# Optimization experiments

Hardware: AMD Instinct MI355X
Metric: run time of the kernel (lower is better)

The kernel has to match this reference:

```python
import jax, jax.numpy as jnp
import numpy as np

EPS = 1e-12  # torch F.normalize eps


def setup_inputs() -> dict:
    key = jax.random.key(0)
    k1, k2, k3 = jax.random.split(key, 3)
    b, c, h, w = 4, 192, 128, 128
    num_heads = 8
    in1 = jax.random.normal(k1, (b, c, h, w), dtype=jnp.float32)
    in2 = jax.random.normal(k2, (b, c, h, w), dtype=jnp.float32)
    scale = jnp.ones((num_heads, 1, 1), dtype=jnp.float32)
    proj_w = jax.random.normal(k3, (c, c), dtype=jnp.float32) * (1.0 / np.sqrt(c))
    return {"in1": in1, "in2": in2, "scale": scale, "proj_w": proj_w, "num_heads": num_heads}


def reference(in1, in2, scale, proj_w, num_heads):
    b, c, h, w = in1.shape
    hd = c // num_heads
    hw = h * w
    # b (head c) h w -> b head c (h w)
    q = in1.reshape(b, num_heads, hd, hw)
    k = in2.reshape(b, num_heads, hd, hw)
    # L2-normalize along the (h w) axis, torch eps semantics
    q = q / jnp.maximum(jnp.linalg.norm(q, axis=-1, keepdims=True), EPS)
    k = k / jnp.maximum(jnp.linalg.norm(k, axis=-1, keepdims=True), EPS)
    # channel-wise attention: [b, head, c, c]
    attn = jnp.einsum('bhcn,bhdn->bhcd', q, k) * scale  # scale broadcasts [head,1,1]
    attn = jax.nn.softmax(attn, axis=-1)
    out = jnp.einsum('bhcd,bhdn->bhcn', attn, k)
    out = out.reshape(b, c, h, w)
    # 1x1 conv projection (no bias)
    out = jnp.einsum('oc,bchw->bohw', proj_w, out)
    return out
```

## Files before the change

### kernel.cpp

```cpp
#include <hip/hip_runtime.h>
#include <hip/hip_bf16.h>
#include <math.h>

#define BATCH 4
#define NHEAD 8
#define HD 24
#define CH 192
#define HW 16384
#define SPL 32
#define SROW 640

#define OFF_MO  (32 * SPL * SROW)
#define OFF_CNT (OFF_MO + (BATCH * CH * CH) / 2)

#define LSTR 132

typedef __attribute__((ext_vector_type(8)))  short bf16x8;
typedef __attribute__((ext_vector_type(16))) float f32x16;

__device__ __forceinline__ unsigned short bf16rne(float x) {
    union { float f; unsigned u; } v; v.f = x;
    unsigned u = v.u;
    return (unsigned short)((u + 0x7FFFu + ((u >> 16) & 1u)) >> 16);
}

__device__ __forceinline__ unsigned pack2(float a, float b) {
    union { __hip_bfloat162 h; unsigned u; } c;
    c.h = __float22bfloat162_rn(float2{a, b});
    return c.u;
}

__device__ __forceinline__ void st_agent(float* p, float v) {
    __hip_atomic_store(p, v, __ATOMIC_RELAXED, __HIP_MEMORY_SCOPE_AGENT);
}
__device__ __forceinline__ float ld_agent(const float* p) {
    return __hip_atomic_load(p, __ATOMIC_RELAXED, __HIP_MEMORY_SCOPE_AGENT);
}

__global__ __launch_bounds__(256, 4) void kA(const float* __restrict__ q,
                                             const float* __restrict__ k,
                                             const float* __restrict__ scale,
                                             const float* __restrict__ w,
                                             float* __restrict__ ws,
                                             unsigned short* __restrict__ Mo,
                                             unsigned int* __restrict__ cnt) {
    __shared__ unsigned int tile[2][HD * LSTR];
    __shared__ int lastFlag;

    const int bh   = blockIdx.x;
    const int ch   = blockIdx.y;
    const int t    = threadIdx.x;
    const int lane = t & 63;
    const int wave = t >> 6;
    const int m    = lane & 31;
    const int hi   = lane >> 5;
    const int rowc = (m < HD) ? m : 0;

    f32x16 aQK = {}, aQQ = {}, aKK = {};

    #pragma unroll
    for (int half = 0; half < 2; ++half) {
        const float* qb = q + (size_t)bh * HD * HW + ch * 512 + half * 256;
        const float* kb = k + (size_t)bh * HD * HW + ch * 512 + half * 256;

        #pragma unroll
        for (int j = 0; j < 6; ++j) {
            const int idx = j * 256 + t;
            const int row = idx >> 6;
            const int c64 = idx & 63;
            float4 qv = *(const float4*)(qb + (size_t)row * HW + c64 * 4);
            float4 kv = *(const float4*)(kb + (size_t)row * HW + c64 * 4);
            *(uint2*)&tile[0][row * LSTR + c64 * 2] =
                make_uint2(pack2(qv.x, qv.y), pack2(qv.z, qv.w));
            *(uint2*)&tile[1][row * LSTR + c64 * 2] =
                make_uint2(pack2(kv.x, kv.y), pack2(kv.z, kv.w));
        }
        __syncthreads();

        #pragma unroll
        for (int s = 0; s < 4; ++s) {
            const int off = (wave * 64 + s * 16) >> 1;
            bf16x8 aq = *(const bf16x8*)&tile[0][rowc * LSTR + off + hi * 4];
            bf16x8 bk = *(const bf16x8*)&tile[1][rowc * LSTR + off + hi * 4];
            aQK = __builtin_amdgcn_mfma_f32_32x32x16_bf16(aq, bk, aQK, 0, 0, 0);
            aQQ = __builtin_amdgcn_mfma_f32_32x32x16_bf16(aq, aq, aQQ, 0, 0, 0);
            aKK = __builtin_amdgcn_mfma_f32_32x32x16_bf16(bk, bk, aKK, 0, 0, 0);
        }
        __syncthreads();
    }

    float* red = (float*)tile;
    if (m < HD) {
        #pragma unroll
        for (int r = 0; r < 16; ++r) {
            const int i = (r & 3) + 8 * (r >> 2) + 4 * hi;
            if (i < HD) {
                red[wave * 624 + i * HD + m] = aQK[r];
                if (i == m) {
                    red[wave * 624 + 576 + i] = aQQ[r];
                    red[wave * 624 + 600 + i] = aKK[r];
                }
            }
        }
    }
    __syncthreads();

    float* Srow = ws + ((size_t)bh * SPL + ch) * SROW;
    for (int e = t; e < 624; e += 256)
        st_agent(&Srow[e], red[e] + red[624 + e] + red[1248 + e] + red[1872 + e]);

    asm volatile("s_waitcnt vmcnt(0)" ::: "memory");
    __syncthreads();

    if (t == 0) {
        unsigned int old = __hip_atomic_fetch_add(&cnt[bh], 1u,
                                                  __ATOMIC_RELAXED,
                                                  __HIP_MEMORY_SCOPE_AGENT);
        lastFlag = (old == SPL - 1);
    }
    __syncthreads();
    if (!lastFlag) return;

    float* sf = (float*)tile;
    const int b = bh >> 3;
    const int h = bh & 7;
    const float* base = ws + (size_t)bh * SPL * SROW;

    for (int idx = t; idx < CH * HD; idx += 256) {
        int o = idx / HD, dd = idx - o * HD;
        sf[672 + idx] = w[o * CH + h * HD + dd];
    }
    for (int e = t; e < 624; e += 256) {
        float s0 = 0.f, s1 = 0.f, s2 = 0.f, s3 = 0.f;
        #pragma unroll
        for (int sp = 0; sp < SPL; sp += 4) {
            s0 += ld_agent(&base[(size_t)(sp + 0) * SROW + e]);
            s1 += ld_agent(&base[(size_t)(sp + 1) * SROW + e]);
            s2 += ld_agent(&base[(size_t)(sp + 2) * SROW + e]);
            s3 += ld_agent(&base[(size_t)(sp + 3) * SROW + e]);
        }
        sf[e] = (s0 + s1) + (s2 + s3);
    }
    __syncthreads();

    if (t < 2 * HD) {
        float inv = 1.0f / fmaxf(sqrtf(sf[576 + t]), 1e-12f);
        sf[624 + t] = inv;
    }
    __syncthreads();

    const float sc = scale[h];
    for (int e = t; e < 576; e += 256)
        sf[e] = sf[e] * sf[624 + e / HD] * sf[648 + e % HD] * sc;
    __syncthreads();

    if (t < HD) {
        float mx = -1e30f;
        for (int j = 0; j < HD; ++j) mx = fmaxf(mx, sf[t * HD + j]);
        float sum = 0.f;
        for (int j = 0; j < HD; ++j) {
            float v = expf(sf[t * HD + j] - mx);
            sf[t * HD + j] = v;
            sum += v;
        }
        float r = 1.0f / sum;
        for (int j = 0; j < HD; ++j) sf[t * HD + j] *= r;
    }
    __syncthreads();

    for (int idx = t; idx < CH * HD; idx += 256) {
        int o = idx / HD, j = idx - o * HD;
        float v = 0.f;
        #pragma unroll
        for (int i = 0; i < HD; ++i)
            v = fmaf(sf[672 + o * HD + i], sf[i * HD + j], v);
        Mo[(size_t)b * CH * CH + (size_t)o * CH + h * HD + j] = bf16rne(v * sf[648 + j]);
    }
}

#define KCN 64
#define BSTR3 100

__global__ __launch_bounds__(256, 4) void kC(const float* __restrict__ k,
                                             const unsigned short* __restrict__ Mo,
                                             float* __restrict__ out) {
    __shared__ unsigned int Bt[KCN * BSTR3];

    const int t    = threadIdx.x;
    const int lane = t & 63;
    const int wave = t >> 6;
    const int n31  = lane & 31;
    const int hi   = lane >> 5;
    const int nt   = wave & 1;
    const int otb  = (wave >> 1) * 3;

    const int nb = blockIdx.x * KCN;
    const int b  = blockIdx.y;

    const float* kb = k + (size_t)b * CH * HW;
    const unsigned short* Mob = Mo + (size_t)b * CH * CH;

    const int np4 = t & 15;
    const int cg4 = t >> 4;

    #pragma unroll
    for (int s = 0; s < 3; ++s) {
        float4 v[4];
        #pragma unroll
        for (int cc = 0; cc < 4; ++cc)
            v[cc] = *(const float4*)(kb + (size_t)(s * 64 + cg4 * 4 + cc) * HW + nb + np4 * 4);
        #pragma unroll
        for (int r = 0; r < 4; ++r) {
            float x0 = (&v[0].x)[r], x1 = (&v[1].x)[r];
            float x2 = (&v[2].x)[r], x3 = (&v[3].x)[r];
            *(uint2*)&Bt[(np4 * 4 + r) * BSTR3 + s * 32 + cg4 * 2] =
                make_uint2(pack2(x0, x1), pack2(x2, x3));
        }
    }
    __syncthreads();

    f32x16 acc[3] = {};
    #pragma unroll
    for (int kc = 0; kc < 12; ++kc) {
        bf16x8 Bf = *(const bf16x8*)&Bt[(nt * 32 + n31) * BSTR3 + kc * 8 + hi * 4];
        #pragma unroll
        for (int oi = 0; oi < 3; ++oi) {
            const unsigned short* ap =
                Mob + (size_t)((otb + oi) * 32 + n31) * CH + kc * 16 + hi * 8;
            bf16x8 Af = *(const bf16x8*)ap;
            acc[oi] = __builtin_amdgcn_mfma_f32_32x32x16_bf16(Af, Bf, acc[oi], 0, 0, 0);
        }
    }

    float* op = out + (size_t)b * CH * HW;
    const int n = nb + nt * 32 + n31;
    #pragma unroll
    for (int oi = 0; oi < 3; ++oi)
        #pragma unroll
        for (int r = 0; r < 16; ++r) {
            int o = (otb + oi) * 32 + (r & 3) + 8 * (r >> 2) + 4 * hi;
            op[(size_t)o * HW + n] = acc[oi][r];
        }
}

extern "C" void kernel_launch(void* const* d_in, const int* in_sizes, int n_in,
                              void* d_out, int out_size, void* d_ws, size_t ws_size,
                              hipStream_t stream) {
    const float* in1   = (const float*)d_in[0];
    const float* in2   = (const float*)d_in[1];
    const float* scale = (const float*)d_in[2];
    const float* projw = (const float*)d_in[3];
    float* ws  = (float*)d_ws;
    float* out = (float*)d_out;
    unsigned short* Mo = (unsigned short*)(ws + OFF_MO);
    unsigned int* cnt  = (unsigned int*)(ws + OFF_CNT);

    hipMemsetAsync((void*)cnt, 0, 32 * sizeof(unsigned int), stream);
    kA<<<dim3(32, SPL), 256, 0, stream>>>(in1, in2, scale, projw, ws, Mo, cnt);
    kC<<<dim3(HW / KCN, BATCH), 256, 0, stream>>>(in2, Mo, out);
}
```

Measured before the change: 174.4 us.

## Software-pipeline global loads with smaller LDS chunks in both kernels

Both kernels now register-prefetch the next chunk of global input while the current chunk is packed to LDS and consumed by MFMAs, instead of loading everything up front and then computing. kA splits its 512-column slice into four 128-column chunks with a smaller LDS tile, and kC streams the 192-channel reduction in three 64-channel stages with a smaller transpose buffer. The aim is to overlap memory latency with compute and to shrink LDS use so more blocks can be resident. In exchange there are more barriers per block and extra live registers for the prefetch buffers.

```diff
diff --git a/kernel.cpp b/kernel.cpp
--- a/kernel.cpp
+++ b/kernel.cpp
@@ -13,7 +13,9 @@
 #define OFF_MO  (32 * SPL * SROW)
 #define OFF_CNT (OFF_MO + (BATCH * CH * CH) / 2)
 
-#define LSTR 132
+#define CHK  128
+#define NCHK 4
+#define ASTR 66
 
 typedef __attribute__((ext_vector_type(8)))  short bf16x8;
 typedef __attribute__((ext_vector_type(16))) float f32x16;
@@ -44,11 +46,12 @@
                                              float* __restrict__ ws,
                                              unsigned short* __restrict__ Mo,
                                              unsigned int* __restrict__ cnt) {
-    __shared__ unsigned int tile[2][HD * LSTR];
+    __shared__ float smem[5280];
+    unsigned int* tile = (unsigned int*)smem;
     __shared__ int lastFlag;
 
     const int bh   = blockIdx.x;
-    const int ch   = blockIdx.y;
+    const int cb   = blockIdx.y;
     const int t    = threadIdx.x;
     const int lane = t & 63;
     const int wave = t >> 6;
@@ -56,40 +59,59 @@
     const int hi   = lane >> 5;
     const int rowc = (m < HD) ? m : 0;
 
+    const float* qb = q + (size_t)bh * HD * HW + cb * 512;
+    const float* kb = k + (size_t)bh * HD * HW + cb * 512;
+
+    int rowj[3], c4j[3];
+    #pragma unroll
+    for (int j = 0; j < 3; ++j) {
+        const int idx = j * 256 + t;
+        rowj[j] = idx >> 5;
+        c4j[j]  = idx & 31;
+    }
+
+    float4 vq[3], vk[3];
+    #pragma unroll
+    for (int j = 0; j < 3; ++j) {
+        vq[j] = *(const float4*)(qb + (size_t)rowj[j] * HW + c4j[j] * 4);
+        vk[j] = *(const float4*)(kb + (size_t)rowj[j] * HW + c4j[j] * 4);
+    }
+
     f32x16 aQK = {}, aQQ = {}, aKK = {};
 
     #pragma unroll
-    for (int half = 0; half < 2; ++half) {
-        const float* qb = q + (size_t)bh * HD * HW + ch * 512 + half * 256;
-        const float* kb = k + (size_t)bh * HD * HW + ch * 512 + half * 256;
-
-        #pragma unroll
-        for (int j = 0; j < 6; ++j) {
-            const int idx = j * 256 + t;
-            const int row = idx >> 6;
-            const int c64 = idx & 63;
-            float4 qv = *(const float4*)(qb + (size_t)row * HW + c64 * 4);
-            float4 kv = *(const float4*)(kb + (size_t)row * HW + c64 * 4);
-            *(uint2*)&tile[0][row * LSTR + c64 * 2] =
-                make_uint2(pack2(qv.x, qv.y), pack2(qv.z, qv.w));
-            *(uint2*)&tile[1][row * LSTR + c64 * 2] =
-                make_uint2(pack2(kv.x, kv.y), pack2(kv.z, kv.w));
+    for (int c = 0; c < NCHK; ++c) {
+        if (c) __syncthreads();
+
+        #pragma unroll
+        for (int j = 0; j < 3; ++j) {
+            *(uint2*)&tile[rowj[j] * ASTR + c4j[j] * 2] =
+                make_uint2(pack2(vq[j].x, vq[j].y), pack2(vq[j].z, vq[j].w));
+            *(uint2*)&tile[24 * ASTR + rowj[j] * ASTR + c4j[j] * 2] =
+                make_uint2(pack2(vk[j].x, vk[j].y), pack2(vk[j].z, vk[j].w));
+        }
+        if (c + 1 < NCHK) {
+            #pragma unroll
+            for (int j = 0; j < 3; ++j) {
+                vq[j] = *(const float4*)(qb + (size_t)rowj[j] * HW + (c + 1) * CHK + c4j[j] * 4);
+                vk[j] = *(const float4*)(kb + (size_t)rowj[j] * HW + (c + 1) * CHK + c4j[j] * 4);
+            }
         }
         __syncthreads();
 
         #pragma unroll
-        for (int s = 0; s < 4; ++s) {
-            const int off = (wave * 64 + s * 16) >> 1;
-            bf16x8 aq = *(const bf16x8*)&tile[0][rowc * LSTR + off + hi * 4];
-            bf16x8 bk = *(const bf16x8*)&tile[1][rowc * LSTR + off + hi * 4];
+        for (int s = 0; s < 2; ++s) {
+            const int off = wave * 16 + s * 8;
+            bf16x8 aq = *(const bf16x8*)&tile[rowc * ASTR + off + hi * 4];
+            bf16x8 bk = *(const bf16x8*)&tile[24 * ASTR + rowc * ASTR + off + hi * 4];
             aQK = __builtin_amdgcn_mfma_f32_32x32x16_bf16(aq, bk, aQK, 0, 0, 0);
             aQQ = __builtin_amdgcn_mfma_f32_32x32x16_bf16(aq, aq, aQQ, 0, 0, 0);
             aKK = __builtin_amdgcn_mfma_f32_32x32x16_bf16(bk, bk, aKK, 0, 0, 0);
         }
-        __syncthreads();
-    }
-
-    float* red = (float*)tile;
+    }
+    __syncthreads();
+
+    float* red = smem;
     if (m < HD) {
         #pragma unroll
         for (int r = 0; r < 16; ++r) {
@@ -105,7 +127,7 @@
     }
     __syncthreads();
 
-    float* Srow = ws + ((size_t)bh * SPL + ch) * SROW;
+    float* Srow = ws + ((size_t)bh * SPL + cb) * SROW;
     for (int e = t; e < 624; e += 256)
         st_agent(&Srow[e], red[e] + red[624 + e] + red[1248 + e] + red[1872 + e]);
 
@@ -121,7 +143,7 @@
     __syncthreads();
     if (!lastFlag) return;
 
-    float* sf = (float*)tile;
+    float* sf = smem;
     const int b = bh >> 3;
     const int h = bh & 7;
     const float* base = ws + (size_t)bh * SPL * SROW;
@@ -179,12 +201,12 @@
 }
 
 #define KCN 64
-#define BSTR3 100
+#define BSTR2 36
 
 __global__ __launch_bounds__(256, 4) void kC(const float* __restrict__ k,
                                              const unsigned short* __restrict__ Mo,
                                              float* __restrict__ out) {
-    __shared__ unsigned int Bt[KCN * BSTR3];
+    __shared__ unsigned int Bt[KCN * BSTR2];
 
     const int t    = threadIdx.x;
     const int lane = t & 63;
@@ -201,34 +223,43 @@
     const unsigned short* Mob = Mo + (size_t)b * CH * CH;
 
     const int np4 = t & 15;
-    const int cg4 = t >> 4;
+    const int cg  = t >> 4;
+
+    float4 v[4];
+    #pragma unroll
+    for (int cc = 0; cc < 4; ++cc)
+        v[cc] = *(const float4*)(kb + (size_t)(cg * 4 + cc) * HW + nb + np4 * 4);
+
+    f32x16 acc[3] = {};
 
     #pragma unroll
     for (int s = 0; s < 3; ++s) {
-        float4 v[4];
-        #pragma unroll
-        for (int cc = 0; cc < 4; ++cc)
-            v[cc] = *(const float4*)(kb + (size_t)(s * 64 + cg4 * 4 + cc) * HW + nb + np4 * 4);
+        if (s) __syncthreads();
+
         #pragma unroll
         for (int r = 0; r < 4; ++r) {
             float x0 = (&v[0].x)[r], x1 = (&v[1].x)[r];
             float x2 = (&v[2].x)[r], x3 = (&v[3].x)[r];
-            *(uint2*)&Bt[(np4 * 4 + r) * BSTR3 + s * 32 + cg4 * 2] =
+            *(uint2*)&Bt[(np4 * 4 + r) * BSTR2 + cg * 2] =
                 make_uint2(pack2(x0, x1), pack2(x2, x3));
         }
-    }
-    __syncthreads();
-
-    f32x16 acc[3] = {};
-    #pragma unroll
-    for (int kc = 0; kc < 12; ++kc) {
-        bf16x8 Bf = *(const bf16x8*)&Bt[(nt * 32 + n31) * BSTR3 + kc * 8 + hi * 4];
-        #pragma unroll
-        for (int oi = 0; oi < 3; ++oi) {
-            const unsigned short* ap =
-                Mob + (size_t)((otb + oi) * 32 + n31) * CH + kc * 16 + hi * 8;
-            bf16x8 Af = *(const bf16x8*)ap;
-            acc[oi] = __builtin_amdgcn_mfma_f32_32x32x16_bf16(Af, Bf, acc[oi], 0, 0, 0);
+        if (s + 1 < 3) {
+            #pragma unroll
+            for (int cc = 0; cc < 4; ++cc)
+                v[cc] = *(const float4*)(kb + (size_t)((s + 1) * 64 + cg * 4 + cc) * HW + nb + np4 * 4);
+        }
+        __syncthreads();
+
+        #pragma unroll
+        for (int kc = 0; kc < 4; ++kc) {
+            bf16x8 Bf = *(const bf16x8*)&Bt[(nt * 32 + n31) * BSTR2 + kc * 8 + hi * 4];
+            #pragma unroll
+            for (int oi = 0; oi < 3; ++oi) {
+                const unsigned short* ap =
+                    Mob + (size_t)((otb + oi) * 32 + n31) * CH + s * 64 + kc * 16 + hi * 8;
+                bf16x8 Af = *(const bf16x8*)ap;
+                acc[oi] = __builtin_amdgcn_mfma_f32_32x32x16_bf16(Af, Bf, acc[oi], 0, 0, 0);
+            }
         }
     }
 
```

Result: no change. 175.8 us (+0.8%).

## Enlarge tiles in both kernels and stage output through LDS for coalesced stores

Applied to the files above, without the earlier changes.

kA now processes 1024 columns per block with half as many splits, and its loads are reorganised so each wave fetches whole rows of q/k into one shared arena. kC grows to 256 columns per block with 512 threads, reloads the k slice in three 64-channel stages, and computes all 192 output rows per wave. Results are transposed through LDS so the output is written as coalesced float4 rows instead of scattered scalar stores. The aim is fewer blocks, more reuse of the Mo loads per block, and better global write efficiency, at the cost of extra barriers and fewer resident blocks per CU.

```diff
diff --git a/kernel.cpp b/kernel.cpp
--- a/kernel.cpp
+++ b/kernel.cpp
@@ -7,13 +7,13 @@
 #define HD 24
 #define CH 192
 #define HW 16384
-#define SPL 32
+#define SPL 16
 #define SROW 640
 
 #define OFF_MO  (32 * SPL * SROW)
 #define OFF_CNT (OFF_MO + (BATCH * CH * CH) / 2)
 
-#define LSTR 132
+#define ASTR 260
 
 typedef __attribute__((ext_vector_type(8)))  short bf16x8;
 typedef __attribute__((ext_vector_type(16))) float f32x16;
@@ -37,18 +37,18 @@
     return __hip_atomic_load(p, __ATOMIC_RELAXED, __HIP_MEMORY_SCOPE_AGENT);
 }
 
-__global__ __launch_bounds__(256, 4) void kA(const float* __restrict__ q,
+__global__ __launch_bounds__(256, 2) void kA(const float* __restrict__ q,
                                              const float* __restrict__ k,
                                              const float* __restrict__ scale,
                                              const float* __restrict__ w,
                                              float* __restrict__ ws,
                                              unsigned short* __restrict__ Mo,
                                              unsigned int* __restrict__ cnt) {
-    __shared__ unsigned int tile[2][HD * LSTR];
+    __shared__ unsigned int arena[48 * ASTR];
     __shared__ int lastFlag;
 
     const int bh   = blockIdx.x;
-    const int ch   = blockIdx.y;
+    const int cb   = blockIdx.y;
     const int t    = threadIdx.x;
     const int lane = t & 63;
     const int wave = t >> 6;
@@ -56,40 +56,54 @@
     const int hi   = lane >> 5;
     const int rowc = (m < HD) ? m : 0;
 
+    const float* qb = q + (size_t)bh * HD * HW + cb * 1024;
+    const float* kb = k + (size_t)bh * HD * HW + cb * 1024;
+
     f32x16 aQK = {}, aQQ = {}, aKK = {};
 
     #pragma unroll
     for (int half = 0; half < 2; ++half) {
-        const float* qb = q + (size_t)bh * HD * HW + ch * 512 + half * 256;
-        const float* kb = k + (size_t)bh * HD * HW + ch * 512 + half * 256;
-
-        #pragma unroll
-        for (int j = 0; j < 6; ++j) {
-            const int idx = j * 256 + t;
-            const int row = idx >> 6;
-            const int c64 = idx & 63;
-            float4 qv = *(const float4*)(qb + (size_t)row * HW + c64 * 4);
-            float4 kv = *(const float4*)(kb + (size_t)row * HW + c64 * 4);
-            *(uint2*)&tile[0][row * LSTR + c64 * 2] =
-                make_uint2(pack2(qv.x, qv.y), pack2(qv.z, qv.w));
-            *(uint2*)&tile[1][row * LSTR + c64 * 2] =
-                make_uint2(pack2(kv.x, kv.y), pack2(kv.z, kv.w));
-        }
-        __syncthreads();
-
-        #pragma unroll
-        for (int s = 0; s < 4; ++s) {
-            const int off = (wave * 64 + s * 16) >> 1;
-            bf16x8 aq = *(const bf16x8*)&tile[0][rowc * LSTR + off + hi * 4];
-            bf16x8 bk = *(const bf16x8*)&tile[1][rowc * LSTR + off + hi * 4];
+        if (half) __syncthreads();
+
+        #pragma unroll
+        for (int grp = 0; grp < 3; ++grp) {
+            float4 v[8];
+            #pragma unroll
+            for (int rr = 0; rr < 4; ++rr) {
+                const int r48 = wave * 12 + grp * 4 + rr;
+                const float* src = (r48 < 24) ? qb : kb;
+                const int row = (r48 < 24) ? r48 : r48 - 24;
+                #pragma unroll
+                for (int i = 0; i < 2; ++i)
+                    v[rr * 2 + i] = *(const float4*)(src + (size_t)row * HW +
+                                                     half * 512 + i * 256 + lane * 4);
+            }
+            #pragma unroll
+            for (int rr = 0; rr < 4; ++rr) {
+                const int r48 = wave * 12 + grp * 4 + rr;
+                #pragma unroll
+                for (int i = 0; i < 2; ++i) {
+                    float4 x = v[rr * 2 + i];
+                    *(uint2*)&arena[r48 * ASTR + i * 128 + lane * 2] =
+                        make_uint2(pack2(x.x, x.y), pack2(x.z, x.w));
+                }
+            }
+        }
+        __syncthreads();
+
+        #pragma unroll
+        for (int s = 0; s < 8; ++s) {
+            const int k16 = wave * 8 + s;
+            bf16x8 aq = *(const bf16x8*)&arena[rowc * ASTR + k16 * 8 + hi * 4];
+            bf16x8 bk = *(const bf16x8*)&arena[(24 + rowc) * ASTR + k16 * 8 + hi * 4];
             aQK = __builtin_amdgcn_mfma_f32_32x32x16_bf16(aq, bk, aQK, 0, 0, 0);
             aQQ = __builtin_amdgcn_mfma_f32_32x32x16_bf16(aq, aq, aQQ, 0, 0, 0);
             aKK = __builtin_amdgcn_mfma_f32_32x32x16_bf16(bk, bk, aKK, 0, 0, 0);
         }
-        __syncthreads();
-    }
-
-    float* red = (float*)tile;
+    }
+    __syncthreads();
+
+    float* red = (float*)arena;
     if (m < HD) {
         #pragma unroll
         for (int r = 0; r < 16; ++r) {
@@ -105,7 +119,7 @@
     }
     __syncthreads();
 
-    float* Srow = ws + ((size_t)bh * SPL + ch) * SROW;
+    float* Srow = ws + ((size_t)bh * SPL + cb) * SROW;
     for (int e = t; e < 624; e += 256)
         st_agent(&Srow[e], red[e] + red[624 + e] + red[1248 + e] + red[1872 + e]);
 
@@ -121,7 +135,7 @@
     __syncthreads();
     if (!lastFlag) return;
 
-    float* sf = (float*)tile;
+    float* sf = (float*)arena;
     const int b = bh >> 3;
     const int h = bh & 7;
     const float* base = ws + (size_t)bh * SPL * SROW;
@@ -178,21 +192,20 @@
     }
 }
 
-#define KCN 64
-#define BSTR3 100
-
-__global__ __launch_bounds__(256, 4) void kC(const float* __restrict__ k,
+#define KCN 256
+#define BSTRC 36
+#define TSTR 260
+
+__global__ __launch_bounds__(512, 2) void kC(const float* __restrict__ k,
                                              const unsigned short* __restrict__ Mo,
                                              float* __restrict__ out) {
-    __shared__ unsigned int Bt[KCN * BSTR3];
+    __shared__ unsigned int arena[KCN * BSTRC];
 
     const int t    = threadIdx.x;
     const int lane = t & 63;
     const int wave = t >> 6;
     const int n31  = lane & 31;
     const int hi   = lane >> 5;
-    const int nt   = wave & 1;
-    const int otb  = (wave >> 1) * 3;
 
     const int nb = blockIdx.x * KCN;
     const int b  = blockIdx.y;
@@ -200,47 +213,55 @@
     const float* kb = k + (size_t)b * CH * HW;
     const unsigned short* Mob = Mo + (size_t)b * CH * CH;
 
-    const int np4 = t & 15;
-    const int cg4 = t >> 4;
+    f32x16 acc[6] = {};
 
     #pragma unroll
     for (int s = 0; s < 3; ++s) {
-        float4 v[4];
-        #pragma unroll
-        for (int cc = 0; cc < 4; ++cc)
-            v[cc] = *(const float4*)(kb + (size_t)(s * 64 + cg4 * 4 + cc) * HW + nb + np4 * 4);
-        #pragma unroll
-        for (int r = 0; r < 4; ++r) {
-            float x0 = (&v[0].x)[r], x1 = (&v[1].x)[r];
-            float x2 = (&v[2].x)[r], x3 = (&v[3].x)[r];
-            *(uint2*)&Bt[(np4 * 4 + r) * BSTR3 + s * 32 + cg4 * 2] =
-                make_uint2(pack2(x0, x1), pack2(x2, x3));
-        }
-    }
-    __syncthreads();
-
-    f32x16 acc[3] = {};
+        if (s) __syncthreads();
+
+        #pragma unroll
+        for (int p = 0; p < 4; ++p) {
+            const int c = s * 64 + wave * 8 + p * 2;
+            float4 a0 = *(const float4*)(kb + (size_t)c * HW + nb + lane * 4);
+            float4 a1 = *(const float4*)(kb + (size_t)(c + 1) * HW + nb + lane * 4);
+            #pragma unroll
+            for (int j = 0; j < 4; ++j)
+                arena[(lane * 4 + j) * BSTRC + wave * 4 + p] =
+                    pack2((&a0.x)[j], (&a1.x)[j]);
+        }
+        __syncthreads();
+
+        #pragma unroll
+        for (int kc = 0; kc < 4; ++kc) {
+            bf16x8 Bf = *(const bf16x8*)&arena[(wave * 32 + n31) * BSTRC + kc * 8 + hi * 4];
+            #pragma unroll
+            for (int oi = 0; oi < 6; ++oi) {
+                const unsigned short* ap =
+                    Mob + (size_t)(oi * 32 + n31) * CH + s * 64 + kc * 16 + hi * 8;
+                bf16x8 Af = *(const bf16x8*)ap;
+                acc[oi] = __builtin_amdgcn_mfma_f32_32x32x16_bf16(Af, Bf, acc[oi], 0, 0, 0);
+            }
+        }
+    }
+
+    float* Tr = (float*)arena;
+    float* op = out + (size_t)b * CH * HW;
     #pragma unroll
-    for (int kc = 0; kc < 12; ++kc) {
-        bf16x8 Bf = *(const bf16x8*)&Bt[(nt * 32 + n31) * BSTR3 + kc * 8 + hi * 4];
-        #pragma unroll
-        for (int oi = 0; oi < 3; ++oi) {
-            const unsigned short* ap =
-                Mob + (size_t)((otb + oi) * 32 + n31) * CH + kc * 16 + hi * 8;
-            bf16x8 Af = *(const bf16x8*)ap;
-            acc[oi] = __builtin_amdgcn_mfma_f32_32x32x16_bf16(Af, Bf, acc[oi], 0, 0, 0);
-        }
-    }
-
-    float* op = out + (size_t)b * CH * HW;
-    const int n = nb + nt * 32 + n31;
-    #pragma unroll
-    for (int oi = 0; oi < 3; ++oi)
+    for (int oi = 0; oi < 6; ++oi) {
+        __syncthreads();
         #pragma unroll
         for (int r = 0; r < 16; ++r) {
-            int o = (otb + oi) * 32 + (r & 3) + 8 * (r >> 2) + 4 * hi;
-            op[(size_t)o * HW + n] = acc[oi][r];
-        }
+            const int orow = (r & 3) + 8 * (r >> 2) + 4 * hi;
+            Tr[orow * TSTR + wave * 32 + n31] = acc[oi][r];
+        }
+        __syncthreads();
+        #pragma unroll
+        for (int rr = 0; rr < 4; ++rr) {
+            const int orow = wave * 4 + rr;
+            float4 val = *(const float4*)&Tr[orow * TSTR + lane * 4];
+            *(float4*)(op + (size_t)(oi * 32 + orow) * HW + nb + lane * 4) = val;
+        }
+    }
 }
 
 extern "C" void kernel_launch(void* const* d_in, const int* in_sizes, int n_in,
@@ -257,5 +278,5 @@
 
     hipMemsetAsync((void*)cnt, 0, 32 * sizeof(unsigned int), stream);
     kA<<<dim3(32, SPL), 256, 0, stream>>>(in1, in2, scale, projw, ws, Mo, cnt);
-    kC<<<dim3(HW / KCN, BATCH), 256, 0, stream>>>(in2, Mo, out);
-}
+    kC<<<dim3(HW / KCN, BATCH), 512, 0, stream>>>(in2, Mo, out);
+}
```

Result: slower. 183.1 us (+5.0%).
